# Kernel optimization log

Hardware: AMD Instinct MI355X
Metric: run time of the kernel (lower is better)

The kernel has to match this reference:

```python
import jax, jax.numpy as jnp
import numpy as np

B, L, H = 32, 4096, 512


def setup_inputs() -> dict:
    key = jax.random.key(0)
    k1, k2, k3, k4 = jax.random.split(key, 4)
    hidden = jax.random.normal(k1, (2, 2, B, H), dtype=jnp.float32)  # (h/c, layers, batch, H)
    encoder_outputs = jax.random.normal(k2, (B, L, H), dtype=jnp.float32)
    W = jax.random.normal(k3, (H, H), dtype=jnp.float32) * (1.0 / np.sqrt(H))
    b = jax.random.normal(k4, (H,), dtype=jnp.float32) * 0.02
    return {"hidden": hidden, "encoder_outputs": encoder_outputs, "W": W, "b": b}


def reference(hidden, encoder_outputs, W, b):
    # hidden[0]: h-state [layers, batch, H] -> transpose(0,1) -> [batch, layers, H] -> last layer
    h_last = hidden[0].transpose(1, 0, 2)[:, -1, :]            # [B, H]
    # method == 'general': energy[b,i] = h_last[b] . (W @ enc[b,i] + b)
    proj = jnp.einsum('blh,oh->blo', encoder_outputs, W) + b   # [B, L, H]
    energies = jnp.einsum('bh,blh->bl', h_last, proj)          # [B, L]
    return jax.nn.softmax(energies, axis=1)[:, None, :]        # [B, 1, L]
```

## Files before the change

### kernel.cpp

```cpp
#include <hip/hip_runtime.h>

#define BATCH 32
#define LSEQ 4096
#define HDIM 512
#define PARTS 4

typedef float f32x4 __attribute__((ext_vector_type(4)));

__global__ __launch_bounds__(512) void proj_kernel(
    const float* __restrict__ hidden, const float* __restrict__ W,
    const float* __restrict__ bias, float* __restrict__ vpart,
    float* __restrict__ cpart)
{
    const int b    = blockIdx.x;
    const int part = blockIdx.y;
    const int h    = threadIdx.x;
    const int OS   = HDIM / PARTS;
    const int obase = part * OS;

    __shared__ float s_hl[HDIM / PARTS];
    if (h < OS) s_hl[h] = hidden[(BATCH + b) * HDIM + obase + h];
    __syncthreads();

    float acc = 0.f;
#pragma unroll 16
    for (int o = 0; o < OS; ++o) {
        acc += s_hl[o] * W[(obase + o) * HDIM + h];
    }
    vpart[(part * BATCH + b) * HDIM + h] = acc;

    float p = (h < OS) ? s_hl[h] * bias[obase + h] : 0.f;
#pragma unroll
    for (int off = 1; off < 64; off <<= 1) p += __shfl_xor(p, off, 64);

    __shared__ float red[8];
    const int wid  = h >> 6;
    const int lane = h & 63;
    if (lane == 0) red[wid] = p;
    __syncthreads();
    if (h == 0) {
        float s = 0.f;
#pragma unroll
        for (int w = 0; w < 8; ++w) s += red[w];
        cpart[part * BATCH + b] = s;
    }
}

__global__ __launch_bounds__(256) void energy_kernel(
    const float* __restrict__ enc, const float* __restrict__ vpart,
    const float* __restrict__ cpart, float* __restrict__ energies)
{
    const int wave = threadIdx.x >> 6;
    const int lane = threadIdx.x & 63;
    const int sub  = lane >> 4;
    const int sl   = lane & 15;

    const int b      = blockIdx.x >> 5;
    const int l_base = (blockIdx.x & 31) * 128 + wave * 32;

    const f32x4* vp0 = (const f32x4*)(vpart + (0 * BATCH + b) * HDIM);
    const f32x4* vp1 = (const f32x4*)(vpart + (1 * BATCH + b) * HDIM);
    const f32x4* vp2 = (const f32x4*)(vpart + (2 * BATCH + b) * HDIM);
    const f32x4* vp3 = (const f32x4*)(vpart + (3 * BATCH + b) * HDIM);
    f32x4 vv[8];
#pragma unroll
    for (int k = 0; k < 8; ++k) {
        const int ch = sl + 16 * k;
        vv[k] = vp0[ch] + vp1[ch] + vp2[ch] + vp3[ch];
    }
    const float cb = cpart[b] + cpart[BATCH + b] + cpart[2 * BATCH + b]
                   + cpart[3 * BATCH + b];

    const long rbase = (long)b * LSEQ + l_base;

#pragma unroll 2
    for (int batch = 0; batch < 8; ++batch) {
        const long r = rbase + batch * 4 + sub;
        const f32x4* ep = (const f32x4*)(enc + r * HDIM) + sl;

        f32x4 e[8];
#pragma unroll
        for (int k = 0; k < 8; ++k)
            e[k] = ep[16 * k];

        float d = 0.f;
#pragma unroll
        for (int k = 0; k < 8; ++k) {
            d += e[k].x * vv[k].x + e[k].y * vv[k].y
               + e[k].z * vv[k].z + e[k].w * vv[k].w;
        }

        d += __shfl_xor(d, 1, 64);
        d += __shfl_xor(d, 2, 64);
        d += __shfl_xor(d, 4, 64);
        d += __shfl_xor(d, 8, 64);

        if (sl == 0) energies[r] = d + cb;
    }
}

__global__ __launch_bounds__(1024) void softmax_kernel(float* __restrict__ out)
{
    const int b = blockIdx.x;
    const int t = threadIdx.x;
    const int wid  = t >> 6;
    const int lane = t & 63;

    float4* o4 = (float4*)(out + (long)b * LSEQ);

    float4 v0 = o4[t];
    float m = fmaxf(fmaxf(v0.x, v0.y), fmaxf(v0.z, v0.w));

    __shared__ float smax[16];
#pragma unroll
    for (int off = 1; off < 64; off <<= 1) m = fmaxf(m, __shfl_xor(m, off, 64));
    if (lane == 0) smax[wid] = m;
    __syncthreads();
#pragma unroll
    for (int w = 0; w < 16; ++w) m = fmaxf(m, smax[w]);

    v0.x = __expf(v0.x - m); v0.y = __expf(v0.y - m);
    v0.z = __expf(v0.z - m); v0.w = __expf(v0.w - m);

    float s = v0.x + v0.y + v0.z + v0.w;
    __shared__ float ssum[16];
#pragma unroll
    for (int off = 1; off < 64; off <<= 1) s += __shfl_xor(s, off, 64);
    if (lane == 0) ssum[wid] = s;
    __syncthreads();
    s = 0.f;
#pragma unroll
    for (int w = 0; w < 16; ++w) s += ssum[w];

    const float inv = 1.0f / s;
    v0.x *= inv; v0.y *= inv; v0.z *= inv; v0.w *= inv;
    o4[t] = v0;
}

extern "C" void kernel_launch(void* const* d_in, const int* in_sizes, int n_in,
                              void* d_out, int out_size, void* d_ws, size_t ws_size,
                              hipStream_t stream)
{
    const float* hidden = (const float*)d_in[0];
    const float* enc    = (const float*)d_in[1];
    const float* W      = (const float*)d_in[2];
    const float* bias   = (const float*)d_in[3];

    float* ws    = (float*)d_ws;
    float* vpart = ws;
    float* cpart = ws + PARTS * BATCH * HDIM;

    float* out = (float*)d_out;

    proj_kernel<<<dim3(BATCH, PARTS), 512, 0, stream>>>(hidden, W, bias, vpart, cpart);
    energy_kernel<<<(BATCH * LSEQ) / 128, 256, 0, stream>>>(enc, vpart, cpart, out);
    softmax_kernel<<<BATCH, 1024, 0, stream>>>(out);
}
```

Measured before the change: 56.38 us.

## Drop softmax-invariant bias term, double energy grid, split dot-product accumulators

The per-batch constant h·b is added equally to every energy in a row, so softmax cancels it. The change deletes its computation and the extra reduction in the projection kernel. The energy kernel now launches twice as many blocks, each covering 64 rows, with a fully unrolled 4-iteration loop and an occupancy hint. It also sums the dot product into four independent accumulators to shorten the FMA dependency chain. The aim is more parallelism and memory-level concurrency on the bandwidth-bound encoder read, at the cost of reloading the v vector in more blocks.

```diff
diff --git a/kernel.cpp b/kernel.cpp
--- a/kernel.cpp
+++ b/kernel.cpp
@@ -9,8 +9,7 @@
 
 __global__ __launch_bounds__(512) void proj_kernel(
     const float* __restrict__ hidden, const float* __restrict__ W,
-    const float* __restrict__ bias, float* __restrict__ vpart,
-    float* __restrict__ cpart)
+    float* __restrict__ vpart)
 {
     const int b    = blockIdx.x;
     const int part = blockIdx.y;
@@ -28,35 +27,19 @@
         acc += s_hl[o] * W[(obase + o) * HDIM + h];
     }
     vpart[(part * BATCH + b) * HDIM + h] = acc;
-
-    float p = (h < OS) ? s_hl[h] * bias[obase + h] : 0.f;
-#pragma unroll
-    for (int off = 1; off < 64; off <<= 1) p += __shfl_xor(p, off, 64);
-
-    __shared__ float red[8];
-    const int wid  = h >> 6;
-    const int lane = h & 63;
-    if (lane == 0) red[wid] = p;
-    __syncthreads();
-    if (h == 0) {
-        float s = 0.f;
-#pragma unroll
-        for (int w = 0; w < 8; ++w) s += red[w];
-        cpart[part * BATCH + b] = s;
-    }
 }
 
-__global__ __launch_bounds__(256) void energy_kernel(
+__global__ __launch_bounds__(256, 5) void energy_kernel(
     const float* __restrict__ enc, const float* __restrict__ vpart,
-    const float* __restrict__ cpart, float* __restrict__ energies)
+    float* __restrict__ energies)
 {
     const int wave = threadIdx.x >> 6;
     const int lane = threadIdx.x & 63;
     const int sub  = lane >> 4;
     const int sl   = lane & 15;
 
-    const int b      = blockIdx.x >> 5;
-    const int l_base = (blockIdx.x & 31) * 128 + wave * 32;
+    const int b      = blockIdx.x >> 6;
+    const int l_base = (blockIdx.x & 63) * 64 + wave * 16;
 
     const f32x4* vp0 = (const f32x4*)(vpart + (0 * BATCH + b) * HDIM);
     const f32x4* vp1 = (const f32x4*)(vpart + (1 * BATCH + b) * HDIM);
@@ -68,13 +51,11 @@
         const int ch = sl + 16 * k;
         vv[k] = vp0[ch] + vp1[ch] + vp2[ch] + vp3[ch];
     }
-    const float cb = cpart[b] + cpart[BATCH + b] + cpart[2 * BATCH + b]
-                   + cpart[3 * BATCH + b];
 
     const long rbase = (long)b * LSEQ + l_base;
 
-#pragma unroll 2
-    for (int batch = 0; batch < 8; ++batch) {
+#pragma unroll
+    for (int batch = 0; batch < 4; ++batch) {
         const long r = rbase + batch * 4 + sub;
         const f32x4* ep = (const f32x4*)(enc + r * HDIM) + sl;
 
@@ -83,19 +64,30 @@
         for (int k = 0; k < 8; ++k)
             e[k] = ep[16 * k];
 
-        float d = 0.f;
-#pragma unroll
-        for (int k = 0; k < 8; ++k) {
-            d += e[k].x * vv[k].x + e[k].y * vv[k].y
-               + e[k].z * vv[k].z + e[k].w * vv[k].w;
-        }
+        float d0 = e[0].x * vv[0].x + e[0].y * vv[0].y
+                 + e[0].z * vv[0].z + e[0].w * vv[0].w;
+        float d1 = e[1].x * vv[1].x + e[1].y * vv[1].y
+                 + e[1].z * vv[1].z + e[1].w * vv[1].w;
+        float d2 = e[2].x * vv[2].x + e[2].y * vv[2].y
+                 + e[2].z * vv[2].z + e[2].w * vv[2].w;
+        float d3 = e[3].x * vv[3].x + e[3].y * vv[3].y
+                 + e[3].z * vv[3].z + e[3].w * vv[3].w;
+        d0 += e[4].x * vv[4].x + e[4].y * vv[4].y
+            + e[4].z * vv[4].z + e[4].w * vv[4].w;
+        d1 += e[5].x * vv[5].x + e[5].y * vv[5].y
+            + e[5].z * vv[5].z + e[5].w * vv[5].w;
+        d2 += e[6].x * vv[6].x + e[6].y * vv[6].y
+            + e[6].z * vv[6].z + e[6].w * vv[6].w;
+        d3 += e[7].x * vv[7].x + e[7].y * vv[7].y
+            + e[7].z * vv[7].z + e[7].w * vv[7].w;
+        float d = (d0 + d1) + (d2 + d3);
 
         d += __shfl_xor(d, 1, 64);
         d += __shfl_xor(d, 2, 64);
         d += __shfl_xor(d, 4, 64);
         d += __shfl_xor(d, 8, 64);
 
-        if (sl == 0) energies[r] = d + cb;
+        if (sl == 0) energies[r] = d;
     }
 }
 
@@ -144,15 +136,13 @@
     const float* hidden = (const float*)d_in[0];
     const float* enc    = (const float*)d_in[1];
     const float* W      = (const float*)d_in[2];
-    const float* bias   = (const float*)d_in[3];
 
     float* ws    = (float*)d_ws;
     float* vpart = ws;
-    float* cpart = ws + PARTS * BATCH * HDIM;
 
     float* out = (float*)d_out;
 
-    proj_kernel<<<dim3(BATCH, PARTS), 512, 0, stream>>>(hidden, W, bias, vpart, cpart);
-    energy_kernel<<<(BATCH * LSEQ) / 128, 256, 0, stream>>>(enc, vpart, cpart, out);
+    proj_kernel<<<dim3(BATCH, PARTS), 512, 0, stream>>>(hidden, W, vpart);
+    energy_kernel<<<(BATCH * LSEQ) / 64, 256, 0, stream>>>(enc, vpart, out);
     softmax_kernel<<<BATCH, 1024, 0, stream>>>(out);
 }
```

After: 53.85 us. 1.05x faster.
